# Performance work log

Hardware: AMD Instinct MI355X
Metric: run time of the kernel (lower is better)

## Reference

```python
import math
import jax, jax.numpy as jnp
import numpy as np

DIM = 256
HEADS = 4
TAU = 1e-3
TOPK = 64


def setup_inputs() -> dict:
    key = jax.random.key(0)
    ks = jax.random.split(key, 11)
    B, N, D = 4, 1024, DIM
    s = 1.0 / math.sqrt(D)
    return {
        "F_cls": jax.random.normal(ks[0], (B, N, D), jnp.float32),
        "F_seg": jax.random.normal(ks[1], (B, N, D), jnp.float32),
        "F_age": jax.random.normal(ks[2], (B, N, D), jnp.float32),
        "Wq": jax.random.normal(ks[3], (D, D), jnp.float32) * s,
        "bq": jnp.zeros((D,), jnp.float32),
        "Wk": jax.random.normal(ks[4], (D, D), jnp.float32) * s,
        "bk": jnp.zeros((D,), jnp.float32),
        "Wv": jax.random.normal(ks[5], (D, D), jnp.float32) * s,
        "bv": jnp.zeros((D,), jnp.float32),
        "Wo": jax.random.normal(ks[6], (D, D), jnp.float32) * s,
        "bo": jnp.zeros((D,), jnp.float32),
    }


def reference(F_cls, F_seg, F_age, Wq, bq, Wk, bk, Wv, bv, Wo, bo):
    # Concatenate the three task branches along tokens: (B, 3N, D)
    X = jnp.concatenate([F_cls, F_seg, F_age], axis=1)
    # L1 soft-thresholding
    Xs = jnp.sign(X) * jnp.maximum(jnp.abs(X) - TAU, 0.0)
    B, TN, D = Xs.shape
    N = F_cls.shape[1]
    H, Dh = HEADS, D // HEADS
    # per-sample channel saliency and top-k channel mask
    sal = jnp.abs(Xs).mean(axis=1)                      # (B, D)
    _, idx = jax.lax.top_k(sal, TOPK)                   # (B, k)
    mask = jnp.zeros((B, D), bool).at[jnp.arange(B)[:, None], idx].set(True)
    Xt = Xs * mask[:, None, :]                          # (B, TN, D)
    # shared K/V over all tokens; Q over all tokens equals the concat of the
    # three per-branch q_proj outputs (same weights), so one fused attention
    # is mathematically identical to the three original calls.
    Q = Xt @ Wq.T + bq
    K = Xt @ Wk.T + bk
    V = Xt @ Wv.T + bv
    def heads(x):
        return x.reshape(B, TN, H, Dh).transpose(0, 2, 1, 3)  # (B,H,TN,Dh)
    Qh, Kh, Vh = heads(Q), heads(K), heads(V)
    logits = jnp.einsum("bhqd,bhkd->bhqk", Qh, Kh) / math.sqrt(Dh)
    A = jax.nn.softmax(logits, axis=-1)
    out = jnp.einsum("bhqk,bhkd->bhqd", A, Vh)
    out = out.transpose(0, 2, 1, 3).reshape(B, TN, D)
    out = out @ Wo.T + bo
    return (out[:, 0:N], out[:, N:2 * N], out[:, 2 * N:3 * N])
```

## Files before the change

kernel.cpp:

```cpp
#include <hip/hip_runtime.h>
#include <math.h>

typedef __attribute__((ext_vector_type(8))) short bf16x8;
typedef __attribute__((ext_vector_type(16))) float f32x16;

#define Bsz 4
#define Nn 1024
#define TN 3072
#define Dd 256
#define Hh 4
#define DH 64
#define TAUc 1e-3f
#define QSCALE 0.1803368801111f

#define SALP_OFF 0
#define IDX_OFF  98304
#define XCB_OFF  98560
#define WCT_OFF  491776
#define QB_OFF   590080
#define KB_OFF   2162944
#define VT_OFF   3735808
#define OP0_OFF  5308672
#define OP1_OFF  8454400
#define SML_OFF  11600128

__device__ __forceinline__ ushort f2b(float f) {
    uint u = __float_as_uint(f);
    u += 0x7fffu + ((u >> 16) & 1u);
    return (ushort)(u >> 16);
}
__device__ __forceinline__ uint pk2(float a, float b) {
    return (uint)f2b(a) | ((uint)f2b(b) << 16);
}
__device__ __forceinline__ uint trunc_pk(float a, float b) {
    return (__float_as_uint(a) >> 16) | (__float_as_uint(b) & 0xFFFF0000u);
}
__device__ __forceinline__ float hi_f(float a) {
    return __uint_as_float(__float_as_uint(a) & 0xFFFF0000u);
}
__device__ __forceinline__ uint cvtpk(float a, float b) {
    uint r;
    asm("v_cvt_pk_bf16_f32 %0, %1, %2" : "=v"(r) : "v"(a), "v"(b));
    return r;
}
__device__ __forceinline__ void gld16(const ushort* g, ushort* l) {
    __builtin_amdgcn_global_load_lds(
        (const __attribute__((address_space(1))) uint*)g,
        (__attribute__((address_space(3))) uint*)l, 16, 0, 0);
}
union U4B8 { uint u[4]; bf16x8 v; };
__device__ __forceinline__ bf16x8 ld8(const ushort* p) { return *(const bf16x8*)p; }

__global__ __launch_bounds__(256) void k_sal(
        const float* __restrict__ F0, const float* __restrict__ F1,
        const float* __restrict__ F2, float* __restrict__ salp) {
    int b = blockIdx.x / 96;
    int slab = blockIdx.x - b * 96;
    int t0 = slab * 32;
    int seg = t0 >> 10, tt0 = t0 & 1023;
    const float* F = (seg == 0) ? F0 : (seg == 1 ? F1 : F2);
    const float* base = &F[(size_t)((b << 10) + tt0) * Dd + threadIdx.x];
    float acc = 0.f;
    #pragma unroll 4
    for (int r = 0; r < 32; ++r) {
        float x = base[(size_t)r * Dd];
        acc += fmaxf(fabsf(x) - TAUc, 0.f);
    }
    salp[blockIdx.x * 256 + threadIdx.x] = acc;
}

__global__ void k_topk(const float* __restrict__ salp, int* __restrict__ idx) {
    __shared__ float v[256];
    __shared__ int cnt;
    int b = blockIdx.x, tid = threadIdx.x;
    float myval = 0.f;
    const float* p = &salp[(size_t)b * 96 * 256 + tid];
    #pragma unroll 4
    for (int s = 0; s < 96; ++s) myval += p[s * 256];
    v[tid] = myval;
    if (tid == 0) cnt = 0;
    __syncthreads();
    for (int k = 2; k <= 256; k <<= 1)
        for (int j = k >> 1; j > 0; j >>= 1) {
            int ixj = tid ^ j;
            if (ixj > tid) {
                float a = v[tid], c = v[ixj];
                bool up = ((tid & k) == 0);
                if ((a > c) == up) { v[tid] = c; v[ixj] = a; }
            }
            __syncthreads();
        }
    float thr = v[192];
    if (myval >= thr) {
        int p2 = atomicAdd(&cnt, 1);
        if (p2 < 64) idx[b * 64 + p2] = tid;
    }
}

__global__ __launch_bounds__(256) void k_gather(
        const float* __restrict__ F0, const float* __restrict__ F1,
        const float* __restrict__ F2,
        const float* __restrict__ Wq, const float* __restrict__ Wk,
        const float* __restrict__ Wv, const int* __restrict__ idx,
        uint* __restrict__ Xcb, uint* __restrict__ Wct) {
    __shared__ float xs[32 * 260];
    __shared__ int ids[64];
    int tid = threadIdx.x;
    if (blockIdx.x < 384) {
        int b = blockIdx.x / 96;
        int t0 = (blockIdx.x - b * 96) * 32;
        if (tid < 64) ids[tid] = idx[b * 64 + tid];
        int seg = t0 >> 10, tt0 = t0 & 1023;
        const float* F = (seg == 0) ? F0 : (seg == 1 ? F1 : F2);
        const float* base = &F[(size_t)((b << 10) + tt0) * Dd];
        #pragma unroll
        for (int i = 0; i < 8; ++i) {
            int i0 = tid + i * 256;
            int r = i0 >> 6, c4 = (i0 & 63) << 2;
            float4 x = *(const float4*)&base[(size_t)r * Dd + c4];
            x.x = copysignf(fmaxf(fabsf(x.x) - TAUc, 0.f), x.x);
            x.y = copysignf(fmaxf(fabsf(x.y) - TAUc, 0.f), x.y);
            x.z = copysignf(fmaxf(fabsf(x.z) - TAUc, 0.f), x.z);
            x.w = copysignf(fmaxf(fabsf(x.w) - TAUc, 0.f), x.w);
            *(float4*)&xs[r * 260 + c4] = x;
        }
        __syncthreads();
        #pragma unroll
        for (int i = 0; i < 4; ++i) {
            int i0 = tid + i * 256;
            int r = i0 >> 5, jp = i0 & 31;
            float x0 = xs[r * 260 + ids[2 * jp]];
            float x1 = xs[r * 260 + ids[2 * jp + 1]];
            Xcb[(size_t)(b * TN + t0 + r) * 32 + jp] = pk2(x0, x1);
        }
    } else {
        int gid = (blockIdx.x - 384) * 256 + tid;
        int b = gid / 24576;
        if (tid < 64) ids[tid] = idx[b * 64 + tid];
        __syncthreads();
        int rem = gid - b * 24576;
        int mat = rem / 8192;
        int rem2 = rem - mat * 8192;
        int dout = rem2 >> 5, jp = rem2 & 31;
        const float* Wm = (mat == 0) ? Wq : (mat == 1 ? Wk : Wv);
        float w0 = Wm[(size_t)dout * 256 + ids[2 * jp]];
        float w1 = Wm[(size_t)dout * 256 + ids[2 * jp + 1]];
        Wct[((size_t)(b * 3 + mat) * 256 + dout) * 32 + jp] = pk2(w0, w1);
    }
}

__global__ __launch_bounds__(256) void k_qkv(
        const ushort* __restrict__ Xcb, const ushort* __restrict__ Wct,
        const float* __restrict__ bq, const float* __restrict__ bk,
        const float* __restrict__ bv,
        ushort* __restrict__ Qh, ushort* __restrict__ Kh, ushort* __restrict__ Vt) {
    int wave = threadIdx.x >> 6, lane = threadIdx.x & 63;
    int l31 = lane & 31, h = lane >> 5;
    int W = blockIdx.x * 4 + wave;
    int b = W / 576;
    int r = W - b * 576;
    int mat = r / 192;
    int p = r - mat * 192;
    const ushort* Xb = Xcb + (size_t)b * TN * 64;
    const ushort* Wm = Wct + (size_t)(b * 3 + mat) * 256 * 64;
    f32x16 c[4];
    #pragma unroll
    for (int nt = 0; nt < 4; ++nt)
        #pragma unroll
        for (int q = 0; q < 16; ++q) c[nt][q] = 0.f;
    if (mat < 2) {
        int mtt = p % 96, ng = p / 96;
        const ushort* arow = &Xb[(size_t)(mtt * 32 + l31) * 64];
        #pragma unroll
        for (int kc = 0; kc < 4; ++kc) {
            bf16x8 af = ld8(arow + kc * 16 + 8 * h);
            #pragma unroll
            for (int nt = 0; nt < 4; ++nt) {
                bf16x8 bf = ld8(&Wm[(size_t)(ng * 128 + nt * 32 + l31) * 64 + kc * 16 + 8 * h]);
                c[nt] = __builtin_amdgcn_mfma_f32_32x32x16_bf16(af, bf, c[nt], 0, 0, 0);
            }
        }
        if (mat == 0) {
            #pragma unroll
            for (int nt = 0; nt < 4; ++nt) {
                int dout = ng * 128 + nt * 32 + l31;
                int head = dout >> 6, d63 = dout & 63;
                float bb = bq[dout];
                size_t obase = ((size_t)(b * 4 + head) * TN + mtt * 32) * 64 + d63;
                #pragma unroll
                for (int u = 0; u < 16; ++u) {
                    int trow = (u & 3) + 8 * (u >> 2) + 4 * h;
                    Qh[obase + (size_t)trow * 64] = f2b((c[nt][u] + bb) * QSCALE);
                }
            }
        } else {
            #pragma unroll
            for (int nt = 0; nt < 4; ++nt) {
                int dout = ng * 128 + nt * 32 + l31;
                int head = dout >> 6, d63 = dout & 63;
                float bb = bk[dout];
                size_t base = (size_t)(b * 4 + head) * 196608;
                #pragma unroll
                for (int u = 0; u < 16; ++u) {
                    int trow = (u & 3) + 8 * (u >> 2) + 4 * h;
                    int t = mtt * 32 + trow;
                    int row = t & 127, tile = t >> 7;
                    int fk = (row ^ (row >> 3)) & 7;
                    Kh[base + (size_t)tile * 8192 + row * 64 +
                       (((d63 >> 3) ^ fk) << 3) + (d63 & 7)] = f2b(c[nt][u] + bb);
                }
            }
        }
    } else {
        int mtv = p & 7, tg = p >> 3;
        const ushort* arow = &Wm[(size_t)(mtv * 32 + l31) * 64];
        #pragma unroll
        for (int kc = 0; kc < 4; ++kc) {
            bf16x8 af = ld8(arow + kc * 16 + 8 * h);
            #pragma unroll
            for (int nt = 0; nt < 4; ++nt) {
                bf16x8 bf = ld8(&Xb[(size_t)(tg * 128 + nt * 32 + l31) * 64 + kc * 16 + 8 * h]);
                c[nt] = __builtin_amdgcn_mfma_f32_32x32x16_bf16(af, bf, c[nt], 0, 0, 0);
            }
        }
        int head = mtv >> 1;
        int sl = (l31 & 19) | ((l31 & 4) << 1) | ((l31 & 8) >> 1);
        size_t vbase = (size_t)(b * 4 + head) * 196608 + (size_t)tg * 8192;
        #pragma unroll
        for (int nt = 0; nt < 4; ++nt) {
            int cc = (nt * 32 + sl) >> 3;
            int elem = sl & 7;
            #pragma unroll
            for (int u = 0; u < 16; ++u) {
                int dout = mtv * 32 + (u & 3) + 8 * (u >> 2) + 4 * h;
                int row = dout & 63;
                int fv = (row ^ (row >> 3)) & 7;
                int ch = (cc & 8) | ((cc & 7) ^ fv);
                Vt[vbase + row * 128 + ch * 8 + elem] = f2b(c[nt][u] + bv[dout]);
            }
        }
    }
}

__global__ __launch_bounds__(256, 3) void k_attn(
        const ushort* __restrict__ Qg, const ushort* __restrict__ Kg,
        const ushort* __restrict__ Vtg,
        float* __restrict__ OP0, float* __restrict__ OP1,
        float* __restrict__ Sml) {
    __shared__ __align__(16) ushort Ks[128 * 64];
    __shared__ __align__(16) ushort Vts[64 * 128];
    int bh = blockIdx.x / 48;
    int rem = blockIdx.x - bh * 48;
    int qt = rem >> 1, ks = rem & 1;
    int b = bh >> 2, hh = bh & 3;
    int tid = threadIdx.x, wave = tid >> 6, lane = tid & 63;
    int l31 = lane & 31, h = lane >> 5;
    int q0 = qt * 128 + wave * 32;
    const ushort* Qb = Qg + ((size_t)bh * TN + q0 + l31) * DH;
    bf16x8 qf[4];
    #pragma unroll
    for (int kc = 0; kc < 4; ++kc) qf[kc] = ld8(&Qb[kc * 16 + 8 * h]);

    const ushort* Kt = Kg + (size_t)bh * 196608 + (size_t)(ks * 12) * 8192 + tid * 8;
    const ushort* Vtt = Vtg + (size_t)bh * 196608 + (size_t)(ks * 12) * 8192 + tid * 8;

    f32x16 o0, o1;
    #pragma unroll
    for (int q = 0; q < 16; ++q) { o0[q] = 0.f; o1[q] = 0.f; }
    float lrun = 0.f;

    int fq0 = (l31 ^ (l31 >> 3)) & 7;
    int fq1 = ((32 + l31) ^ ((32 + l31) >> 3)) & 7;

    #pragma unroll 1
    for (int it = 0; it < 12; ++it) {
        __syncthreads();
        #pragma unroll
        for (int i = 0; i < 4; ++i) {
            gld16(Kt + i * 2048, &Ks[(tid + i * 256) * 8]);
            gld16(Vtt + i * 2048, &Vts[(tid + i * 256) * 8]);
        }
        Kt += 8192; Vtt += 8192;
        __syncthreads();

        uint pkA[32];
        float psum = 0.f;
        #pragma unroll
        for (int hf = 0; hf < 2; ++hf) {
            f32x16 s0, s1;
            #pragma unroll
            for (int q = 0; q < 16; ++q) { s0[q] = 0.f; s1[q] = 0.f; }
            int r0 = hf * 64 + l31, r1 = r0 + 32;
            #pragma unroll
            for (int kc = 0; kc < 4; ++kc) {
                int ch = 2 * kc + h;
                bf16x8 k0 = ld8(&Ks[r0 * 64 + ((ch ^ fq0) << 3)]);
                bf16x8 k1 = ld8(&Ks[r1 * 64 + ((ch ^ fq1) << 3)]);
                s0 = __builtin_amdgcn_mfma_f32_32x32x16_bf16(k0, qf[kc], s0, 0, 0, 0);
                s1 = __builtin_amdgcn_mfma_f32_32x32x16_bf16(k1, qf[kc], s1, 0, 0, 0);
            }
            #pragma unroll
            for (int u = 0; u < 8; ++u) {
                float pa = exp2f(s0[2 * u]), pb = exp2f(s0[2 * u + 1]);
                psum += pa + pb;
                pkA[hf * 16 + u] = cvtpk(pa, pb);
            }
            #pragma unroll
            for (int u = 0; u < 8; ++u) {
                float pa = exp2f(s1[2 * u]), pb = exp2f(s1[2 * u + 1]);
                psum += pa + pb;
                pkA[hf * 16 + 8 + u] = cvtpk(pa, pb);
            }
        }
        psum += __shfl_xor(psum, 32);
        lrun += psum;

        #pragma unroll
        for (int kc2 = 0; kc2 < 8; ++kc2) {
            U4B8 pf;
            pf.u[0] = pkA[4 * kc2];     pf.u[1] = pkA[4 * kc2 + 1];
            pf.u[2] = pkA[4 * kc2 + 2]; pf.u[3] = pkA[4 * kc2 + 3];
            int ch = 2 * kc2 + h;
            bf16x8 v0f = ld8(&Vts[l31 * 128 + (((ch & 8) | ((ch & 7) ^ fq0)) << 3)]);
            bf16x8 v1f = ld8(&Vts[(32 + l31) * 128 + (((ch & 8) | ((ch & 7) ^ fq1)) << 3)]);
            o0 = __builtin_amdgcn_mfma_f32_32x32x16_bf16(pf.v, v0f, o0, 0, 0, 0);
            o1 = __builtin_amdgcn_mfma_f32_32x32x16_bf16(pf.v, v1f, o1, 0, 0, 0);
        }
    }

    float* OP = ks ? OP1 : OP0;
    #pragma unroll
    for (int q = 0; q < 16; ++q) {
        int qrow = (q & 3) + 8 * (q >> 2) + 4 * h;
        int t = q0 + qrow;
        size_t base = ((size_t)b * TN + t) * Dd + hh * 64;
        OP[base + l31] = o0[q];
        OP[base + 32 + l31] = o1[q];
    }
    if (h == 0)
        Sml[(size_t)ks * 49152 + (size_t)bh * TN + q0 + l31] = lrun;
}

__global__ __launch_bounds__(256) void k_out(
        const float* __restrict__ OP0, const float* __restrict__ OP1,
        const float* __restrict__ Sml, const float* __restrict__ Wo,
        const float* __restrict__ bo, float* __restrict__ out) {
    __shared__ __align__(16) ushort Ms[2][64][64];
    __shared__ float invsh[64 * 4];
    int nd4 = blockIdx.x;
    int R0 = blockIdx.y * 64;
    int b = R0 / TN;
    int tloc0 = R0 - b * TN;
    int tid = threadIdx.x, wave = tid >> 6, lane = tid & 63;
    int l31 = lane & 31, h = lane >> 5;
    int wt = wave & 1, wd = wave >> 1;
    {
        int hd = tid >> 6, t = tid & 63;
        size_t o = (size_t)(b * 4 + hd) * TN + tloc0 + t;
        invsh[t * 4 + hd] = 1.f / (Sml[o] + Sml[49152 + o]);
    }
    int dout = nd4 * 64 + wd * 32 + l31;
    float bb = bo[dout];
    const float* wrow = &Wo[(size_t)dout * 256];
    int st_t = tid >> 2, st_c = tid & 3;
    int fst = (st_t ^ (st_t >> 3)) & 7;
    size_t gbase = ((size_t)(b * TN + tloc0 + st_t)) * 256 + st_c * 8;
    int trow = wt * 32 + l31;
    int ftr = (trow ^ (trow >> 3)) & 7;
    f32x16 acc;
    #pragma unroll
    for (int q = 0; q < 16; ++q) acc[q] = 0.f;

    auto stage_load = [&](int st, int buf) {
        size_t ob = gbase + (size_t)st * 32;
        float4 x0 = *(const float4*)&OP0[ob];
        float4 x1 = *(const float4*)&OP0[ob + 4];
        float4 y0 = *(const float4*)&OP1[ob];
        float4 y1 = *(const float4*)&OP1[ob + 4];
        float s = invsh[st_t * 4 + (st >> 1)];
        float m0 = (x0.x + y0.x) * s, m1 = (x0.y + y0.y) * s;
        float m2 = (x0.z + y0.z) * s, m3 = (x0.w + y0.w) * s;
        float m4 = (x1.x + y1.x) * s, m5 = (x1.y + y1.y) * s;
        float m6 = (x1.z + y1.z) * s, m7 = (x1.w + y1.w) * s;
        uint4 hi = { trunc_pk(m0, m1), trunc_pk(m2, m3),
                     trunc_pk(m4, m5), trunc_pk(m6, m7) };
        uint4 lo = { trunc_pk(m0 - hi_f(m0), m1 - hi_f(m1)),
                     trunc_pk(m2 - hi_f(m2), m3 - hi_f(m3)),
                     trunc_pk(m4 - hi_f(m4), m5 - hi_f(m5)),
                     trunc_pk(m6 - hi_f(m6), m7 - hi_f(m7)) };
        *(uint4*)&Ms[buf][st_t][(st_c ^ fst) * 8] = hi;
        *(uint4*)&Ms[buf][st_t][((4 + st_c) ^ fst) * 8] = lo;
    };

    __syncthreads();
    stage_load(0, 0);
    #pragma unroll 1
    for (int st = 0; st < 8; ++st) {
        __syncthreads();
        if (st < 7) stage_load(st + 1, (st + 1) & 1);
        int buf = st & 1;
        #pragma unroll
        for (int kc = 0; kc < 2; ++kc) {
            bf16x8 ah = *(const bf16x8*)&Ms[buf][trow][((2 * kc + h) ^ ftr) * 8];
            bf16x8 al = *(const bf16x8*)&Ms[buf][trow][((4 + 2 * kc + h) ^ ftr) * 8];
            int din0 = st * 32 + kc * 16 + 8 * h;
            float4 w0 = *(const float4*)&wrow[din0];
            float4 w1 = *(const float4*)&wrow[din0 + 4];
            U4B8 wh, wl;
            wh.u[0] = trunc_pk(w0.x, w0.y); wh.u[1] = trunc_pk(w0.z, w0.w);
            wh.u[2] = trunc_pk(w1.x, w1.y); wh.u[3] = trunc_pk(w1.z, w1.w);
            wl.u[0] = trunc_pk(w0.x - hi_f(w0.x), w0.y - hi_f(w0.y));
            wl.u[1] = trunc_pk(w0.z - hi_f(w0.z), w0.w - hi_f(w0.w));
            wl.u[2] = trunc_pk(w1.x - hi_f(w1.x), w1.y - hi_f(w1.y));
            wl.u[3] = trunc_pk(w1.z - hi_f(w1.z), w1.w - hi_f(w1.w));
            acc = __builtin_amdgcn_mfma_f32_32x32x16_bf16(ah, wh.v, acc, 0, 0, 0);
            acc = __builtin_amdgcn_mfma_f32_32x32x16_bf16(al, wh.v, acc, 0, 0, 0);
            acc = __builtin_amdgcn_mfma_f32_32x32x16_bf16(ah, wl.v, acc, 0, 0, 0);
        }
    }
    #pragma unroll
    for (int u = 0; u < 16; ++u) {
        int tloc = tloc0 + wt * 32 + (u & 3) + 8 * (u >> 2) + 4 * h;
        int chunk = tloc >> 10, tt = tloc & 1023;
        out[(size_t)chunk * (Bsz * Nn * Dd) + ((size_t)(b * Nn + tt)) * Dd + dout] =
            acc[u] + bb;
    }
}

extern "C" void kernel_launch(void* const* d_in, const int* in_sizes, int n_in,
                              void* d_out, int out_size, void* d_ws, size_t ws_size,
                              hipStream_t stream) {
    const float* F0 = (const float*)d_in[0];
    const float* F1 = (const float*)d_in[1];
    const float* F2 = (const float*)d_in[2];
    const float* Wq = (const float*)d_in[3];
    const float* bq = (const float*)d_in[4];
    const float* Wk = (const float*)d_in[5];
    const float* bk = (const float*)d_in[6];
    const float* Wv = (const float*)d_in[7];
    const float* bv = (const float*)d_in[8];
    const float* Wo = (const float*)d_in[9];
    const float* bo = (const float*)d_in[10];
    float* ws = (float*)d_ws;
    float* out = (float*)d_out;

    int* idxp = (int*)(ws + IDX_OFF);
    uint* Xcb = (uint*)(ws + XCB_OFF);
    uint* Wct = (uint*)(ws + WCT_OFF);
    ushort* Qb16 = (ushort*)(ws + QB_OFF);
    ushort* Kb16 = (ushort*)(ws + KB_OFF);
    ushort* Vt16 = (ushort*)(ws + VT_OFF);
    float* OP0 = ws + OP0_OFF;
    float* OP1 = ws + OP1_OFF;
    float* Sml = ws + SML_OFF;

    k_sal<<<384, 256, 0, stream>>>(F0, F1, F2, ws + SALP_OFF);
    k_topk<<<Bsz, 256, 0, stream>>>(ws + SALP_OFF, idxp);
    k_gather<<<768, 256, 0, stream>>>(F0, F1, F2, Wq, Wk, Wv, idxp, Xcb, Wct);
    k_qkv<<<576, 256, 0, stream>>>((const ushort*)Xcb, (const ushort*)Wct,
                                   bq, bk, bv, Qb16, Kb16, Vt16);
    k_attn<<<768, 256, 0, stream>>>(Qb16, Kb16, Vt16, OP0, OP1, Sml);
    k_out<<<dim3(4, 192), 256, 0, stream>>>(OP0, OP1, Sml, Wo, bo, out);
}
```

Measured before the change: 187.8 us.

## Split attention keys four ways with atomic accumulation into a single output buffer

Attention now splits the key range into four chunks instead of two, doubling the grid to 1536 blocks and raising the occupancy hint to 4. Partial outputs and row sums are combined with float atomic adds into one buffer that earlier kernels zero, replacing the two separate partial buffers. The row sum is now produced by an extra MFMA against a vector of ones instead of a scalar sum and shuffle. The changes aim at more parallelism and less partial-buffer traffic in the output kernel, but they add atomic contention, an extra MFMA per step and non-deterministic summation order.

```diff
diff --git a/kernel.cpp b/kernel.cpp
--- a/kernel.cpp
+++ b/kernel.cpp
@@ -20,9 +20,8 @@
 #define QB_OFF   590080
 #define KB_OFF   2162944
 #define VT_OFF   3735808
-#define OP0_OFF  5308672
-#define OP1_OFF  8454400
-#define SML_OFF  11600128
+#define OP_OFF   5308672
+#define SML_OFF  8454400
 
 __device__ __forceinline__ ushort f2b(float f) {
     uint u = __float_as_uint(f);
@@ -53,7 +52,14 @@
 
 __global__ __launch_bounds__(256) void k_sal(
         const float* __restrict__ F0, const float* __restrict__ F1,
-        const float* __restrict__ F2, float* __restrict__ salp) {
+        const float* __restrict__ F2, float* __restrict__ salp,
+        float* __restrict__ OPz) {
+    {
+        size_t zb = ((size_t)blockIdx.x * 256 + threadIdx.x) * 32;
+        float4 z = {0.f, 0.f, 0.f, 0.f};
+        #pragma unroll
+        for (int i = 0; i < 8; ++i) *(float4*)&OPz[zb + i * 4] = z;
+    }
     int b = blockIdx.x / 96;
     int slab = blockIdx.x - b * 96;
     int t0 = slab * 32;
@@ -69,10 +75,19 @@
     salp[blockIdx.x * 256 + threadIdx.x] = acc;
 }
 
-__global__ void k_topk(const float* __restrict__ salp, int* __restrict__ idx) {
+__global__ void k_topk(const float* __restrict__ salp, int* __restrict__ idx,
+                       float* __restrict__ Smlz) {
     __shared__ float v[256];
     __shared__ int cnt;
     int b = blockIdx.x, tid = threadIdx.x;
+    {
+        int gid = b * 256 + tid;
+        #pragma unroll
+        for (int i = 0; i < 12; ++i) {
+            float4 z = {0.f, 0.f, 0.f, 0.f};
+            *(float4*)&Smlz[(size_t)gid * 48 + i * 4] = z;
+        }
+    }
     float myval = 0.f;
     const float* p = &salp[(size_t)b * 96 * 256 + tid];
     #pragma unroll 4
@@ -242,16 +257,15 @@
     }
 }
 
-__global__ __launch_bounds__(256, 3) void k_attn(
+__global__ __launch_bounds__(256, 4) void k_attn(
         const ushort* __restrict__ Qg, const ushort* __restrict__ Kg,
         const ushort* __restrict__ Vtg,
-        float* __restrict__ OP0, float* __restrict__ OP1,
-        float* __restrict__ Sml) {
+        float* __restrict__ OP, float* __restrict__ Sml) {
     __shared__ __align__(16) ushort Ks[128 * 64];
     __shared__ __align__(16) ushort Vts[64 * 128];
-    int bh = blockIdx.x / 48;
-    int rem = blockIdx.x - bh * 48;
-    int qt = rem >> 1, ks = rem & 1;
+    int bh = blockIdx.x / 96;
+    int rem = blockIdx.x - bh * 96;
+    int qt = rem >> 2, ks = rem & 3;
     int b = bh >> 2, hh = bh & 3;
     int tid = threadIdx.x, wave = tid >> 6, lane = tid & 63;
     int l31 = lane & 31, h = lane >> 5;
@@ -261,19 +275,21 @@
     #pragma unroll
     for (int kc = 0; kc < 4; ++kc) qf[kc] = ld8(&Qb[kc * 16 + 8 * h]);
 
-    const ushort* Kt = Kg + (size_t)bh * 196608 + (size_t)(ks * 12) * 8192 + tid * 8;
-    const ushort* Vtt = Vtg + (size_t)bh * 196608 + (size_t)(ks * 12) * 8192 + tid * 8;
-
-    f32x16 o0, o1;
-    #pragma unroll
-    for (int q = 0; q < 16; ++q) { o0[q] = 0.f; o1[q] = 0.f; }
-    float lrun = 0.f;
+    const ushort* Kt = Kg + (size_t)bh * 196608 + (size_t)(ks * 6) * 8192 + tid * 8;
+    const ushort* Vtt = Vtg + (size_t)bh * 196608 + (size_t)(ks * 6) * 8192 + tid * 8;
+
+    f32x16 o0, o1, lacc;
+    #pragma unroll
+    for (int q = 0; q < 16; ++q) { o0[q] = 0.f; o1[q] = 0.f; lacc[q] = 0.f; }
+    U4B8 ones;
+    ones.u[0] = 0x3F803F80u; ones.u[1] = 0x3F803F80u;
+    ones.u[2] = 0x3F803F80u; ones.u[3] = 0x3F803F80u;
 
     int fq0 = (l31 ^ (l31 >> 3)) & 7;
     int fq1 = ((32 + l31) ^ ((32 + l31) >> 3)) & 7;
 
     #pragma unroll 1
-    for (int it = 0; it < 12; ++it) {
+    for (int it = 0; it < 6; ++it) {
         __syncthreads();
         #pragma unroll
         for (int i = 0; i < 4; ++i) {
@@ -284,7 +300,6 @@
         __syncthreads();
 
         uint pkA[32];
-        float psum = 0.f;
         #pragma unroll
         for (int hf = 0; hf < 2; ++hf) {
             f32x16 s0, s1;
@@ -300,20 +315,12 @@
                 s1 = __builtin_amdgcn_mfma_f32_32x32x16_bf16(k1, qf[kc], s1, 0, 0, 0);
             }
             #pragma unroll
-            for (int u = 0; u < 8; ++u) {
-                float pa = exp2f(s0[2 * u]), pb = exp2f(s0[2 * u + 1]);
-                psum += pa + pb;
-                pkA[hf * 16 + u] = cvtpk(pa, pb);
-            }
-            #pragma unroll
-            for (int u = 0; u < 8; ++u) {
-                float pa = exp2f(s1[2 * u]), pb = exp2f(s1[2 * u + 1]);
-                psum += pa + pb;
-                pkA[hf * 16 + 8 + u] = cvtpk(pa, pb);
-            }
-        }
-        psum += __shfl_xor(psum, 32);
-        lrun += psum;
+            for (int u = 0; u < 8; ++u)
+                pkA[hf * 16 + u] = cvtpk(exp2f(s0[2 * u]), exp2f(s0[2 * u + 1]));
+            #pragma unroll
+            for (int u = 0; u < 8; ++u)
+                pkA[hf * 16 + 8 + u] = cvtpk(exp2f(s1[2 * u]), exp2f(s1[2 * u + 1]));
+        }
 
         #pragma unroll
         for (int kc2 = 0; kc2 < 8; ++kc2) {
@@ -325,26 +332,31 @@
             bf16x8 v1f = ld8(&Vts[(32 + l31) * 128 + (((ch & 8) | ((ch & 7) ^ fq1)) << 3)]);
             o0 = __builtin_amdgcn_mfma_f32_32x32x16_bf16(pf.v, v0f, o0, 0, 0, 0);
             o1 = __builtin_amdgcn_mfma_f32_32x32x16_bf16(pf.v, v1f, o1, 0, 0, 0);
-        }
-    }
-
-    float* OP = ks ? OP1 : OP0;
+            lacc = __builtin_amdgcn_mfma_f32_32x32x16_bf16(pf.v, ones.v, lacc, 0, 0, 0);
+        }
+    }
+
     #pragma unroll
     for (int q = 0; q < 16; ++q) {
         int qrow = (q & 3) + 8 * (q >> 2) + 4 * h;
         int t = q0 + qrow;
         size_t base = ((size_t)b * TN + t) * Dd + hh * 64;
-        OP[base + l31] = o0[q];
-        OP[base + 32 + l31] = o1[q];
-    }
-    if (h == 0)
-        Sml[(size_t)ks * 49152 + (size_t)bh * TN + q0 + l31] = lrun;
+        unsafeAtomicAdd(&OP[base + l31], o0[q]);
+        unsafeAtomicAdd(&OP[base + 32 + l31], o1[q]);
+    }
+    if (l31 == 0) {
+        #pragma unroll
+        for (int u = 0; u < 16; ++u) {
+            int qrow = (u & 3) + 8 * (u >> 2) + 4 * h;
+            unsafeAtomicAdd(&Sml[(size_t)bh * TN + q0 + qrow], lacc[u]);
+        }
+    }
 }
 
 __global__ __launch_bounds__(256) void k_out(
-        const float* __restrict__ OP0, const float* __restrict__ OP1,
-        const float* __restrict__ Sml, const float* __restrict__ Wo,
-        const float* __restrict__ bo, float* __restrict__ out) {
+        const float* __restrict__ OP, const float* __restrict__ Sml,
+        const float* __restrict__ Wo, const float* __restrict__ bo,
+        float* __restrict__ out) {
     __shared__ __align__(16) ushort Ms[2][64][64];
     __shared__ float invsh[64 * 4];
     int nd4 = blockIdx.x;
@@ -356,8 +368,7 @@
     int wt = wave & 1, wd = wave >> 1;
     {
         int hd = tid >> 6, t = tid & 63;
-        size_t o = (size_t)(b * 4 + hd) * TN + tloc0 + t;
-        invsh[t * 4 + hd] = 1.f / (Sml[o] + Sml[49152 + o]);
+        invsh[t * 4 + hd] = 1.f / Sml[(size_t)(b * 4 + hd) * TN + tloc0 + t];
     }
     int dout = nd4 * 64 + wd * 32 + l31;
     float bb = bo[dout];
@@ -373,15 +384,11 @@
 
     auto stage_load = [&](int st, int buf) {
         size_t ob = gbase + (size_t)st * 32;
-        float4 x0 = *(const float4*)&OP0[ob];
-        float4 x1 = *(const float4*)&OP0[ob + 4];
-        float4 y0 = *(const float4*)&OP1[ob];
-        float4 y1 = *(const float4*)&OP1[ob + 4];
+        float4 x0 = *(const float4*)&OP[ob];
+        float4 x1 = *(const float4*)&OP[ob + 4];
         float s = invsh[st_t * 4 + (st >> 1)];
-        float m0 = (x0.x + y0.x) * s, m1 = (x0.y + y0.y) * s;
-        float m2 = (x0.z + y0.z) * s, m3 = (x0.w + y0.w) * s;
-        float m4 = (x1.x + y1.x) * s, m5 = (x1.y + y1.y) * s;
-        float m6 = (x1.z + y1.z) * s, m7 = (x1.w + y1.w) * s;
+        float m0 = x0.x * s, m1 = x0.y * s, m2 = x0.z * s, m3 = x0.w * s;
+        float m4 = x1.x * s, m5 = x1.y * s, m6 = x1.z * s, m7 = x1.w * s;
         uint4 hi = { trunc_pk(m0, m1), trunc_pk(m2, m3),
                      trunc_pk(m4, m5), trunc_pk(m6, m7) };
         uint4 lo = { trunc_pk(m0 - hi_f(m0), m1 - hi_f(m1)),
@@ -450,15 +457,14 @@
     ushort* Qb16 = (ushort*)(ws + QB_OFF);
     ushort* Kb16 = (ushort*)(ws + KB_OFF);
     ushort* Vt16 = (ushort*)(ws + VT_OFF);
-    float* OP0 = ws + OP0_OFF;
-    float* OP1 = ws + OP1_OFF;
+    float* OP = ws + OP_OFF;
     float* Sml = ws + SML_OFF;
 
-    k_sal<<<384, 256, 0, stream>>>(F0, F1, F2, ws + SALP_OFF);
-    k_topk<<<Bsz, 256, 0, stream>>>(ws + SALP_OFF, idxp);
+    k_sal<<<384, 256, 0, stream>>>(F0, F1, F2, ws + SALP_OFF, OP);
+    k_topk<<<Bsz, 256, 0, stream>>>(ws + SALP_OFF, idxp, Sml);
     k_gather<<<768, 256, 0, stream>>>(F0, F1, F2, Wq, Wk, Wv, idxp, Xcb, Wct);
     k_qkv<<<576, 256, 0, stream>>>((const ushort*)Xcb, (const ushort*)Wct,
                                    bq, bk, bv, Qb16, Kb16, Vt16);
-    k_attn<<<768, 256, 0, stream>>>(Qb16, Kb16, Vt16, OP0, OP1, Sml);
-    k_out<<<dim3(4, 192), 256, 0, stream>>>(OP0, OP1, Sml, Wo, bo, out);
-}
+    k_attn<<<1536, 256, 0, stream>>>(Qb16, Kb16, Vt16, OP, Sml);
+    k_out<<<dim3(4, 192), 256, 0, stream>>>(OP, Sml, Wo, bo, out);
+}
```

After: 245.4 us. 30.7% more time.
